# Performance work log

Measured on AMD Instinct MI355X. Metric: run time of the kernel, lower is better.

## Reference

```python
import jax, jax.numpy as jnp
import numpy as np

S, D, H, F = 4096, 2048, 16, 8192
HD = D // H
EPS = 1e-5


def setup_inputs() -> dict:
    key = jax.random.key(0)
    ks = jax.random.split(key, 16)
    sc_d = 1.0 / np.sqrt(D)
    sc_f = 1.0 / np.sqrt(F)
    return {
        "x": jax.random.normal(ks[0], (S, D), dtype=jnp.float32),
        # stacked per-head projections: [H, D, HD]
        "Wq": jax.random.normal(ks[1], (H, D, HD), dtype=jnp.float32) * sc_d,
        "bq": jax.random.normal(ks[2], (H, HD), dtype=jnp.float32) * 0.01,
        "Wk": jax.random.normal(ks[3], (H, D, HD), dtype=jnp.float32) * sc_d,
        "bk": jax.random.normal(ks[4], (H, HD), dtype=jnp.float32) * 0.01,
        "Wv": jax.random.normal(ks[5], (H, D, HD), dtype=jnp.float32) * sc_d,
        "bv": jax.random.normal(ks[6], (H, HD), dtype=jnp.float32) * 0.01,
        "Wp": jax.random.normal(ks[7], (D, D), dtype=jnp.float32) * sc_d,
        "bp": jax.random.normal(ks[8], (D,), dtype=jnp.float32) * 0.01,
        "W1": jax.random.normal(ks[9], (D, F), dtype=jnp.float32) * sc_d,
        "b1": jax.random.normal(ks[10], (F,), dtype=jnp.float32) * 0.01,
        "W2": jax.random.normal(ks[11], (F, D), dtype=jnp.float32) * sc_f,
        "b2": jax.random.normal(ks[12], (D,), dtype=jnp.float32) * 0.01,
        "gamma": jnp.ones((D,), dtype=jnp.float32),
        "beta": jnp.zeros((D,), dtype=jnp.float32),
    }


def _layernorm(x, gamma, beta):
    mu = jnp.mean(x, axis=-1, keepdims=True)
    var = jnp.var(x, axis=-1, keepdims=True)
    return (x - mu) * jax.lax.rsqrt(var + EPS) * gamma + beta


def reference(x, Wq, bq, Wk, bk, Wv, bv, Wp, bp, W1, b1, W2, b2, gamma, beta):
    residual = x
    # batched per-head projections: [H, S, HD]
    q = jnp.einsum('sd,hde->hse', x, Wq) + bq[:, None, :]
    k = jnp.einsum('sd,hde->hse', x, Wk) + bk[:, None, :]
    v = jnp.einsum('sd,hde->hse', x, Wv) + bv[:, None, :]
    scores = jnp.einsum('hse,hte->hst', q, k) / np.sqrt(HD).astype(np.float32)
    attn = jax.nn.softmax(scores, axis=-1)
    heads = jnp.einsum('hst,hte->hse', attn, v)  # [H, S, HD]
    # concat heads along feature dim (head 0 first): [S, H*HD]
    heads = jnp.transpose(heads, (1, 0, 2)).reshape(S, H * HD)
    out = heads @ Wp + bp
    # residual_attn=True, norm_attn=True
    out = out + residual
    out = _layernorm(out, gamma, beta)
    # feedforward (original forward ends here)
    out = jax.nn.relu(out @ W1 + b1) @ W2 + b2
    return out
```

## Files before the change

### kernel.cpp

```cpp
#include <hip/hip_runtime.h>
#include <hip/hip_bf16.h>
#include <cstdint>
#include <cstddef>

#define S 4096
#define D 2048
#define H 16
#define HD 128
#define F 8192

typedef unsigned short ushort_t;
typedef __attribute__((ext_vector_type(8))) short short8;
typedef __attribute__((ext_vector_type(4))) float floatx4;

__device__ __forceinline__ ushort_t f2bf(float f) {
  union { float f; unsigned u; } v; v.f = f;
  unsigned u = v.u;
  return (ushort_t)((u + 0x7fffu + ((u >> 16) & 1u)) >> 16);
}

__device__ __forceinline__ void async16(void* lds, const void* g) {
  __builtin_amdgcn_global_load_lds(
      (const __attribute__((address_space(1))) unsigned int*)g,
      (__attribute__((address_space(3))) unsigned int*)lds, 16, 0, 0);
}

template <int N>
__device__ __forceinline__ void vmcnt_() {
  static_assert(N >= 0 && N <= 4, "vmcnt range");
  if constexpr (N == 0) asm volatile("s_waitcnt vmcnt(0)" ::: "memory");
  else if constexpr (N == 1) asm volatile("s_waitcnt vmcnt(1)" ::: "memory");
  else if constexpr (N == 2) asm volatile("s_waitcnt vmcnt(2)" ::: "memory");
  else if constexpr (N == 3) asm volatile("s_waitcnt vmcnt(3)" ::: "memory");
  else asm volatile("s_waitcnt vmcnt(4)" ::: "memory");
}
__device__ __forceinline__ void bar_() { asm volatile("s_barrier" ::: "memory"); }


__global__ void cast_bf16(const float* __restrict__ src, ushort_t* __restrict__ dst, int n4) {
  int i = blockIdx.x * blockDim.x + threadIdx.x;
  if (i < n4) {
    float4 v = ((const float4*)src)[i];
    ushort4 o;
    o.x = f2bf(v.x); o.y = f2bf(v.y); o.z = f2bf(v.z); o.w = f2bf(v.w);
    ((ushort4*)dst)[i] = o;
  }
}

__global__ void build_bqkv(const float* __restrict__ bq, const float* __restrict__ bk,
                           const float* __restrict__ bv, float* __restrict__ bqkv) {
  int n = blockIdx.x * blockDim.x + threadIdx.x;
  if (n < 3 * D) {
    float v;
    if (n < D) v = bq[n];
    else if (n < 2 * D) v = bk[n - D];
    else v = bv[n - 2 * D];
    bqkv[n] = v;
  }
}

__global__ void transpose_f32_bf16(const float* __restrict__ src, ushort_t* __restrict__ dst,
                                   int ldS, int ldD, long srcBatchStride, long dstBatchRows) {
  __shared__ float t[32][33];
  int b = blockIdx.z;
  src += (size_t)b * srcBatchStride;
  dst += (size_t)b * dstBatchRows * ldD;
  int r0 = blockIdx.x * 32, c0 = blockIdx.y * 32;
  int tx = threadIdx.x, ty = threadIdx.y;
#pragma unroll
  for (int i = 0; i < 4; ++i)
    t[ty + i * 8][tx] = src[(size_t)(r0 + ty + i * 8) * ldS + c0 + tx];
  __syncthreads();
#pragma unroll
  for (int i = 0; i < 4; ++i)
    dst[(size_t)(c0 + ty + i * 8) * ldD + r0 + tx] = f2bf(t[tx][ty + i * 8]);
}

__global__ void transpose_bf16(const ushort_t* __restrict__ src, ushort_t* __restrict__ dst,
                               int ldS, int ldD, int colOff) {
  __shared__ ushort_t t[32][33];
  int r0 = blockIdx.x * 32, c0 = blockIdx.y * 32;
  int tx = threadIdx.x, ty = threadIdx.y;
#pragma unroll
  for (int i = 0; i < 4; ++i)
    t[ty + i * 8][tx] = src[(size_t)(r0 + ty + i * 8) * ldS + colOff + c0 + tx];
  __syncthreads();
#pragma unroll
  for (int i = 0; i < 4; ++i)
    dst[(size_t)(c0 + ty + i * 8) * ldD + r0 + tx] = t[tx][ty + i * 8];
}

template <int MODE, int BM>
__global__ __launch_bounds__(512, 2)
void gemm8p(const ushort_t* __restrict__ A, const ushort_t* __restrict__ Bt,
            const float* __restrict__ bias, const float* __restrict__ resid,
            ushort_t* __restrict__ outb, float* __restrict__ outf,
            int M, int N, int K, int gridN) {
  constexpr int MF = BM / 64;
  constexpr int LA = BM / 128;
  constexpr int AT = BM * 64;
  constexpr int BT = 256 * 64;
  __shared__ __align__(16) ushort_t Abuf[2][AT];
  __shared__ __align__(16) ushort_t Bbuf[2][BT];

  const int tid = threadIdx.x;
  const int l = tid & 63, w = tid >> 6;
  const int c16 = l & 15, g = l >> 4;
  const int wr2 = w >> 2, wc4 = w & 3;

  const int nwg = gridDim.x;
  const int q8 = nwg >> 3, r8 = nwg & 7;
  const int xcd = blockIdx.x & 7, bix = blockIdx.x >> 3;
  const int wgid = (xcd < r8 ? xcd * (q8 + 1) : r8 * (q8 + 1) + (xcd - r8) * q8) + bix;
  const int m0 = (wgid / gridN) * BM;
  const int n0 = (wgid % gridN) * 256;

  const size_t Kb = (size_t)K * 2;

  const char* aSrc[LA]; char* aLds[LA];
#pragma unroll
  for (int i = 0; i < LA; ++i) {
    int ch = i * 512 + tid;
    int row = ch >> 3;
    int slot = ((ch ^ row) & 7) << 4;
    aSrc[i] = (const char*)A + (size_t)(m0 + row) * Kb + slot;
    aLds[i] = (char*)(&Abuf[0][0]) + ch * 16;
  }
  const char* bSrc[2]; char* bLds[2];
#pragma unroll
  for (int i = 0; i < 2; ++i) {
    int ch = i * 512 + tid;
    int row = ch >> 3;
    int slot = ((ch ^ row) & 7) << 4;
    bSrc[i] = (const char*)Bt + (size_t)(n0 + row) * Kb + slot;
    bLds[i] = (char*)(&Bbuf[0][0]) + ch * 16;
  }
  const size_t aHalf = (size_t)(BM / 2) * Kb;
  const size_t bHalf = (size_t)128 * Kb;

  int rdK[2];
  rdK[0] = ((g ^ (c16 & 7)) << 4);
  rdK[1] = (((4 + g) ^ (c16 & 7)) << 4);
  const int aRd = wr2 * (BM / 4) * 128 + c16 * 128;
  const int bRd = wc4 * 32 * 128 + c16 * 128;

  floatx4 acc[2][2][MF][2];
#pragma unroll
  for (int mh = 0; mh < 2; ++mh)
#pragma unroll
    for (int nh = 0; nh < 2; ++nh)
#pragma unroll
      for (int mf = 0; mf < MF; ++mf)
#pragma unroll
        for (int nf = 0; nf < 2; ++nf) acc[mh][nh][mf][nf] = (floatx4){0.f, 0.f, 0.f, 0.f};

  const int NT = K >> 6;

#pragma unroll
  for (int i = 0; i < LA; ++i) async16(aLds[i], aSrc[i]);
#pragma unroll
  for (int i = 0; i < 2; ++i) async16(bLds[i], bSrc[i]);
#pragma unroll
  for (int i = 0; i < 2; ++i) async16(bLds[i] + 128 * 128, bSrc[i] + bHalf);
#pragma unroll
  for (int i = 0; i < LA; ++i) async16(aLds[i] + (BM / 2) * 128, aSrc[i] + aHalf);
  vmcnt_<2 + LA>();
  bar_();

  for (int T = 0; T < NT; ++T) {
    const int kb = T & 1, kn = kb ^ 1;
    const bool last = (T == NT - 1);
    const size_t kOff = (size_t)(T + 1) << 7;
    const char* ab = (const char*)(&Abuf[0][0]) + kb * (AT * 2);
    const char* bb = (const char*)(&Bbuf[0][0]) + kb * (BT * 2);
    const int aOf = kn * (AT * 2), bOf = kn * (BT * 2);
    short8 af[MF][2], bf0[2][2], bf1[2][2];

#pragma unroll
    for (int mf = 0; mf < MF; ++mf)
#pragma unroll
      for (int kk = 0; kk < 2; ++kk)
        af[mf][kk] = *(const short8*)(ab + aRd + mf * 2048 + rdK[kk]);
#pragma unroll
    for (int nf = 0; nf < 2; ++nf)
#pragma unroll
      for (int kk = 0; kk < 2; ++kk)
        bf0[nf][kk] = *(const short8*)(bb + bRd + nf * 2048 + rdK[kk]);
    if (!last) {
#pragma unroll
      for (int i = 0; i < LA; ++i) async16(aLds[i] + aOf, aSrc[i] + kOff);
    }
    bar_();
    __builtin_amdgcn_s_setprio(1);
#pragma unroll
    for (int mf = 0; mf < MF; ++mf)
#pragma unroll
      for (int nf = 0; nf < 2; ++nf)
#pragma unroll
        for (int kk = 0; kk < 2; ++kk)
          acc[0][0][mf][nf] = __builtin_amdgcn_mfma_f32_16x16x32_bf16(
              af[mf][kk], bf0[nf][kk], acc[0][0][mf][nf], 0, 0, 0);
    __builtin_amdgcn_s_setprio(0);
    __builtin_amdgcn_sched_barrier(0);
    if (!last) vmcnt_<2 * LA>(); else vmcnt_<LA>();
    bar_();

#pragma unroll
    for (int nf = 0; nf < 2; ++nf)
#pragma unroll
      for (int kk = 0; kk < 2; ++kk)
        bf1[nf][kk] = *(const short8*)(bb + bRd + 16384 + nf * 2048 + rdK[kk]);
    if (!last) {
#pragma unroll
      for (int i = 0; i < 2; ++i) async16(bLds[i] + bOf, bSrc[i] + kOff);
    }
    bar_();
    __builtin_amdgcn_s_setprio(1);
#pragma unroll
    for (int mf = 0; mf < MF; ++mf)
#pragma unroll
      for (int nf = 0; nf < 2; ++nf)
#pragma unroll
        for (int kk = 0; kk < 2; ++kk)
          acc[0][1][mf][nf] = __builtin_amdgcn_mfma_f32_16x16x32_bf16(
              af[mf][kk], bf1[nf][kk], acc[0][1][mf][nf], 0, 0, 0);
    __builtin_amdgcn_s_setprio(0);
    __builtin_amdgcn_sched_barrier(0);
    if (!last) vmcnt_<LA + 2>(); else vmcnt_<0>();
    bar_();

#pragma unroll
    for (int mf = 0; mf < MF; ++mf)
#pragma unroll
      for (int kk = 0; kk < 2; ++kk)
        af[mf][kk] = *(const short8*)(ab + aRd + (BM / 2) * 128 + mf * 2048 + rdK[kk]);
    if (!last) {
#pragma unroll
      for (int i = 0; i < 2; ++i) async16(bLds[i] + bOf + 16384, bSrc[i] + bHalf + kOff);
    }
    bar_();
    __builtin_amdgcn_s_setprio(1);
#pragma unroll
    for (int mf = 0; mf < MF; ++mf)
#pragma unroll
      for (int nf = 0; nf < 2; ++nf)
#pragma unroll
        for (int kk = 0; kk < 2; ++kk)
          acc[1][1][mf][nf] = __builtin_amdgcn_mfma_f32_16x16x32_bf16(
              af[mf][kk], bf1[nf][kk], acc[1][1][mf][nf], 0, 0, 0);
    __builtin_amdgcn_s_setprio(0);
    __builtin_amdgcn_sched_barrier(0);
    bar_();

    if (!last) {
#pragma unroll
      for (int i = 0; i < LA; ++i) async16(aLds[i] + aOf + (BM / 2) * 128, aSrc[i] + aHalf + kOff);
    }
    bar_();
    __builtin_amdgcn_s_setprio(1);
#pragma unroll
    for (int mf = 0; mf < MF; ++mf)
#pragma unroll
      for (int nf = 0; nf < 2; ++nf)
#pragma unroll
        for (int kk = 0; kk < 2; ++kk)
          acc[1][0][mf][nf] = __builtin_amdgcn_mfma_f32_16x16x32_bf16(
              af[mf][kk], bf0[nf][kk], acc[1][0][mf][nf], 0, 0, 0);
    __builtin_amdgcn_s_setprio(0);
    __builtin_amdgcn_sched_barrier(0);
    if (!last) vmcnt_<2 + LA>();
    bar_();
  }

  const int mBase = m0 + wr2 * (BM / 4) + g * 4;
  const int nBase = n0 + wc4 * 32 + c16;
#pragma unroll
  for (int mh = 0; mh < 2; ++mh)
#pragma unroll
    for (int nh = 0; nh < 2; ++nh)
#pragma unroll
      for (int nf = 0; nf < 2; ++nf) {
        int gcol = nBase + nh * 128 + nf * 16;
        float bj = bias[gcol];
#pragma unroll
        for (int mf = 0; mf < MF; ++mf) {
          int grow = mBase + mh * (BM / 2) + mf * 16;
#pragma unroll
          for (int r = 0; r < 4; ++r) {
            float v = acc[mh][nh][mf][nf][r] + bj;
            size_t o = (size_t)(grow + r) * N + gcol;
            if (MODE == 0) {
              outb[o] = f2bf(v);
            } else if (MODE == 1) {
              outf[o] = v + resid[o];
            } else if (MODE == 2) {
              outb[o] = f2bf(v > 0.f ? v : 0.f);
            } else {
              outf[o] = v;
            }
          }
        }
      }
}

__global__ __launch_bounds__(256, 2)
void attn_kernel(const ushort_t* __restrict__ QKV, const ushort_t* __restrict__ Vt,
                 ushort_t* __restrict__ heads) {
  const int h = blockIdx.y;
  const int tid = threadIdx.x, w = tid >> 6, l = tid & 63;
  const int g = l >> 4, c = l & 15;
  const int q0 = blockIdx.x * 128 + w * 32;
  const float scale = 0.08838834764831845f;

  __shared__ __align__(16) ushort_t Ks[64 * 128];
  __shared__ __align__(16) ushort_t Vs[128 * 64];
  __shared__ __align__(16) ushort_t Ps[4][2][16][72];

  short8 qf[2][4];
#pragma unroll
  for (int u = 0; u < 2; ++u)
#pragma unroll
    for (int k0 = 0; k0 < 4; ++k0)
      qf[u][k0] = *(const short8*)(QKV + (size_t)(q0 + u * 16 + c) * (3 * D) + h * HD + k0 * 32 + g * 8);

  floatx4 o[2][8];
#pragma unroll
  for (int u = 0; u < 2; ++u)
#pragma unroll
    for (int j = 0; j < 8; ++j) o[u][j] = (floatx4){0.f, 0.f, 0.f, 0.f};
  float l_run[2] = {0.f, 0.f};

  for (int t0 = 0; t0 < S; t0 += 64) {
#pragma unroll
    for (int cc = 0; cc < 4; ++cc) {
      int slot = cc * 256 + tid;
      int krow = slot >> 4, kch = slot & 15;
      const char* gk = (const char*)QKV +
          ((size_t)(t0 + krow) * (3 * D) + D + h * HD) * 2 + ((kch ^ (krow & 15)) << 4);
      async16((char*)Ks + (size_t)(cc * 256 + w * 64) * 16, gk);
      int vrow = slot >> 3, vch = slot & 7;
      const char* gv = (const char*)Vt +
          ((size_t)(h * HD + vrow) * S + t0) * 2 + ((vch ^ (vrow & 7)) << 4);
      async16((char*)Vs + (size_t)(cc * 256 + w * 64) * 16, gv);
    }
    __syncthreads();

    floatx4 sc[2][4];
#pragma unroll
    for (int u = 0; u < 2; ++u)
#pragma unroll
      for (int tt = 0; tt < 4; ++tt) sc[u][tt] = (floatx4){0.f, 0.f, 0.f, 0.f};
#pragma unroll
    for (int tt = 0; tt < 4; ++tt) {
      short8 kf[4];
#pragma unroll
      for (int k0 = 0; k0 < 4; ++k0)
        kf[k0] = *(const short8*)(Ks + (tt * 16 + c) * 128 + (((k0 * 4 + g) ^ c) << 3));
#pragma unroll
      for (int u = 0; u < 2; ++u)
#pragma unroll
        for (int k0 = 0; k0 < 4; ++k0)
          sc[u][tt] = __builtin_amdgcn_mfma_f32_16x16x32_bf16(kf[k0], qf[u][k0], sc[u][tt], 0, 0, 0);
    }

#pragma unroll
    for (int u = 0; u < 2; ++u) {
#pragma unroll
      for (int tt = 0; tt < 4; ++tt) {
        float p0 = __expf(sc[u][tt][0] * scale);
        float p1 = __expf(sc[u][tt][1] * scale);
        float p2 = __expf(sc[u][tt][2] * scale);
        float p3 = __expf(sc[u][tt][3] * scale);
        l_run[u] += p0 + p1 + p2 + p3;
        ushort4 pk;
        pk.x = f2bf(p0); pk.y = f2bf(p1); pk.z = f2bf(p2); pk.w = f2bf(p3);
        *reinterpret_cast<ushort4*>(&Ps[w][u][c][tt * 16 + g * 4]) = pk;
      }
    }
    __asm__ volatile("s_waitcnt lgkmcnt(0)" ::: "memory");

    short8 pf[2][2];
#pragma unroll
    for (int u = 0; u < 2; ++u)
#pragma unroll
      for (int tk = 0; tk < 2; ++tk)
        pf[u][tk] = *reinterpret_cast<const short8*>(&Ps[w][u][c][tk * 32 + g * 8]);
#pragma unroll
    for (int j = 0; j < 8; ++j) {
#pragma unroll
      for (int tk = 0; tk < 2; ++tk) {
        short8 vf = *(const short8*)(Vs + (j * 16 + c) * 64 + (((tk * 4 + g) ^ (c & 7)) << 3));
#pragma unroll
        for (int u = 0; u < 2; ++u)
          o[u][j] = __builtin_amdgcn_mfma_f32_16x16x32_bf16(pf[u][tk], vf, o[u][j], 0, 0, 0);
      }
    }
    __syncthreads();
  }

#pragma unroll
  for (int u = 0; u < 2; ++u) {
    float lt = l_run[u];
    lt += __shfl_xor(lt, 16);
    lt += __shfl_xor(lt, 32);
    float linv[4];
#pragma unroll
    for (int r = 0; r < 4; ++r) linv[r] = 1.f / __shfl(lt, g * 4 + r);
    ushort_t* hp = heads + (size_t)(q0 + u * 16 + g * 4) * D + h * HD + c;
#pragma unroll
    for (int j = 0; j < 8; ++j)
#pragma unroll
      for (int r = 0; r < 4; ++r)
        hp[(size_t)r * D + j * 16] = f2bf(o[u][j][r] * linv[r]);
  }
}

__global__ __launch_bounds__(256)
void ln_kernel(const float* __restrict__ preln, const float* __restrict__ gamma,
               const float* __restrict__ beta, ushort_t* __restrict__ y) {
  int row = blockIdx.x, tid = threadIdx.x;
  const float* p = preln + (size_t)row * D;
  float vals[8];
  float sum = 0.f, ss = 0.f;
#pragma unroll
  for (int k = 0; k < 8; ++k) {
    float v = p[tid + k * 256];
    vals[k] = v; sum += v; ss += v * v;
  }
#pragma unroll
  for (int off = 32; off >= 1; off >>= 1) {
    sum += __shfl_xor(sum, off);
    ss += __shfl_xor(ss, off);
  }
  __shared__ float s1[4], s2[4];
  int w = tid >> 6, l = tid & 63;
  if (l == 0) { s1[w] = sum; s2[w] = ss; }
  __syncthreads();
  sum = s1[0] + s1[1] + s1[2] + s1[3];
  ss = s2[0] + s2[1] + s2[2] + s2[3];
  float mu = sum / (float)D;
  float var = ss / (float)D - mu * mu;
  float rs = rsqrtf(var + 1e-5f);
  ushort_t* yr = y + (size_t)row * D;
#pragma unroll
  for (int k = 0; k < 8; ++k) {
    int d = tid + k * 256;
    yr[d] = f2bf((vals[k] - mu) * rs * gamma[d] + beta[d]);
  }
}


extern "C" void kernel_launch(void* const* d_in, const int* in_sizes, int n_in,
                              void* d_out, int out_size, void* d_ws, size_t ws_size,
                              hipStream_t stream) {
  const float* x = (const float*)d_in[0];
  const float* Wq = (const float*)d_in[1];
  const float* bq = (const float*)d_in[2];
  const float* Wk = (const float*)d_in[3];
  const float* bk = (const float*)d_in[4];
  const float* Wv = (const float*)d_in[5];
  const float* bv = (const float*)d_in[6];
  const float* Wp = (const float*)d_in[7];
  const float* bp = (const float*)d_in[8];
  const float* W1 = (const float*)d_in[9];
  const float* b1 = (const float*)d_in[10];
  const float* W2 = (const float*)d_in[11];
  const float* b2 = (const float*)d_in[12];
  const float* gamma = (const float*)d_in[13];
  const float* beta = (const float*)d_in[14];

  char* ws = (char*)d_ws;
  ushort_t* WQKVT = (ushort_t*)(ws + 0);
  ushort_t* XB    = (ushort_t*)(ws + 25165824);
  float*    BQKV  = (float*)(ws + 41943040);
  ushort_t* WPT   = (ushort_t*)(ws + 41975808);
  ushort_t* W1T   = (ushort_t*)(ws + 50364416);
  ushort_t* W2T   = (ushort_t*)(ws + 83918848);
  ushort_t* QKV   = (ushort_t*)(ws + 117473280);
  ushort_t* HEADS = (ushort_t*)(ws + 167804928);
  ushort_t* VT    = (ushort_t*)(ws + 184582144);
  float*    PRELN = (float*)(ws + 0);
  ushort_t* AB    = (ushort_t*)(ws + 117473280);
  ushort_t* Y     = (ushort_t*)(ws + 184582144);
  float* OUT = (float*)d_out;

  dim3 tb(32, 8);
  cast_bf16<<<(S * D / 4 + 255) / 256, 256, 0, stream>>>(x, XB, S * D / 4);
  build_bqkv<<<(3 * D + 255) / 256, 256, 0, stream>>>(bq, bk, bv, BQKV);
  transpose_f32_bf16<<<dim3(D / 32, HD / 32, H), tb, 0, stream>>>(Wq, WQKVT, HD, D, (long)D * HD, HD);
  transpose_f32_bf16<<<dim3(D / 32, HD / 32, H), tb, 0, stream>>>(Wk, WQKVT + (size_t)D * D, HD, D, (long)D * HD, HD);
  transpose_f32_bf16<<<dim3(D / 32, HD / 32, H), tb, 0, stream>>>(Wv, WQKVT + (size_t)2 * D * D, HD, D, (long)D * HD, HD);
  transpose_f32_bf16<<<dim3(D / 32, D / 32, 1), tb, 0, stream>>>(Wp, WPT, D, D, 0, 0);
  transpose_f32_bf16<<<dim3(D / 32, F / 32, 1), tb, 0, stream>>>(W1, W1T, F, D, 0, 0);
  transpose_f32_bf16<<<dim3(F / 32, D / 32, 1), tb, 0, stream>>>(W2, W2T, D, F, 0, 0);
  gemm8p<0, 256><<<dim3((S / 256) * (3 * D / 256)), 512, 0, stream>>>(
      XB, WQKVT, BQKV, nullptr, QKV, nullptr, S, 3 * D, D, 3 * D / 256);
  transpose_bf16<<<dim3(S / 32, D / 32), tb, 0, stream>>>(QKV, VT, 3 * D, S, 2 * D);
  attn_kernel<<<dim3(S / 128, H), 256, 0, stream>>>(QKV, VT, HEADS);
  gemm8p<1, 128><<<dim3((S / 128) * (D / 256)), 512, 0, stream>>>(
      HEADS, WPT, bp, x, nullptr, PRELN, S, D, D, D / 256);
  ln_kernel<<<S, 256, 0, stream>>>(PRELN, gamma, beta, Y);
  gemm8p<2, 256><<<dim3((S / 256) * (F / 256)), 512, 0, stream>>>(
      Y, W1T, b1, nullptr, AB, nullptr, S, F, D, F / 256);
  gemm8p<3, 128><<<dim3((S / 128) * (D / 256)), 512, 0, stream>>>(
      AB, W2T, b2, nullptr, nullptr, OUT, S, D, F, D / 256);
}
```

Baseline: 959.0 us.

## Restructure bf16 GEMM main loop into two-tile unrolled deeper prefetch pipeline

Rewrites the gemm8p main loop to process two K-tiles per iteration with both LDS buffers preloaded up front. Each quarter-tile region is refilled from global memory for tile k+2 as soon as its fragments are read into registers, which lengthens the prefetch distance and is meant to hide global load latency. Explicit lgkmcnt(0) waits with scheduling barriers are added before each MFMA block. The extra waits and barriers could cost some issue overlap, and the loop now assumes K is a multiple of 128.

```diff
diff --git a/kernel.cpp b/kernel.cpp
--- a/kernel.cpp
+++ b/kernel.cpp
@@ -27,14 +27,22 @@
 
 template <int N>
 __device__ __forceinline__ void vmcnt_() {
-  static_assert(N >= 0 && N <= 4, "vmcnt range");
+  static_assert(N >= 0 && N <= 8, "vmcnt range");
   if constexpr (N == 0) asm volatile("s_waitcnt vmcnt(0)" ::: "memory");
   else if constexpr (N == 1) asm volatile("s_waitcnt vmcnt(1)" ::: "memory");
   else if constexpr (N == 2) asm volatile("s_waitcnt vmcnt(2)" ::: "memory");
   else if constexpr (N == 3) asm volatile("s_waitcnt vmcnt(3)" ::: "memory");
-  else asm volatile("s_waitcnt vmcnt(4)" ::: "memory");
+  else if constexpr (N == 4) asm volatile("s_waitcnt vmcnt(4)" ::: "memory");
+  else if constexpr (N == 5) asm volatile("s_waitcnt vmcnt(5)" ::: "memory");
+  else if constexpr (N == 6) asm volatile("s_waitcnt vmcnt(6)" ::: "memory");
+  else if constexpr (N == 7) asm volatile("s_waitcnt vmcnt(7)" ::: "memory");
+  else asm volatile("s_waitcnt vmcnt(8)" ::: "memory");
 }
 __device__ __forceinline__ void bar_() { asm volatile("s_barrier" ::: "memory"); }
+__device__ __forceinline__ void lgkm0_() {
+  asm volatile("s_waitcnt lgkmcnt(0)" ::: "memory");
+  __builtin_amdgcn_sched_barrier(0);
+}
 
 
 __global__ void cast_bf16(const float* __restrict__ src, ushort_t* __restrict__ dst, int n4) {
@@ -96,17 +104,15 @@
             const float* __restrict__ bias, const float* __restrict__ resid,
             ushort_t* __restrict__ outb, float* __restrict__ outf,
             int M, int N, int K, int gridN) {
-  constexpr int MF = BM / 64;
+  constexpr int MQ = BM / 64;
   constexpr int LA = BM / 128;
-  constexpr int AT = BM * 64;
-  constexpr int BT = 256 * 64;
-  __shared__ __align__(16) ushort_t Abuf[2][AT];
-  __shared__ __align__(16) ushort_t Bbuf[2][BT];
+  __shared__ __align__(16) ushort_t Abuf[2][BM * 64];
+  __shared__ __align__(16) ushort_t Bbuf[2][256 * 64];
 
   const int tid = threadIdx.x;
   const int l = tid & 63, w = tid >> 6;
   const int c16 = l & 15, g = l >> 4;
-  const int wr2 = w >> 2, wc4 = w & 3;
+  const int wm = w >> 2, wn = w & 3;
 
   const int nwg = gridDim.x;
   const int q8 = nwg >> 3, r8 = nwg & 7;
@@ -116,14 +122,15 @@
   const int n0 = (wgid % gridN) * 256;
 
   const size_t Kb = (size_t)K * 2;
+  const size_t aHalfB = (size_t)(BM / 2) * Kb;
+  const size_t bHalfB = (size_t)128 * Kb;
 
   const char* aSrc[LA]; char* aLds[LA];
 #pragma unroll
   for (int i = 0; i < LA; ++i) {
     int ch = i * 512 + tid;
     int row = ch >> 3;
-    int slot = ((ch ^ row) & 7) << 4;
-    aSrc[i] = (const char*)A + (size_t)(m0 + row) * Kb + slot;
+    aSrc[i] = (const char*)A + (size_t)(m0 + row) * Kb + (((ch ^ row) & 7) << 4);
     aLds[i] = (char*)(&Abuf[0][0]) + ch * 16;
   }
   const char* bSrc[2]; char* bLds[2];
@@ -131,163 +138,149 @@
   for (int i = 0; i < 2; ++i) {
     int ch = i * 512 + tid;
     int row = ch >> 3;
-    int slot = ((ch ^ row) & 7) << 4;
-    bSrc[i] = (const char*)Bt + (size_t)(n0 + row) * Kb + slot;
+    bSrc[i] = (const char*)Bt + (size_t)(n0 + row) * Kb + (((ch ^ row) & 7) << 4);
     bLds[i] = (char*)(&Bbuf[0][0]) + ch * 16;
   }
-  const size_t aHalf = (size_t)(BM / 2) * Kb;
-  const size_t bHalf = (size_t)128 * Kb;
+
+  auto stA = [&](int p, int h, int kByte) {
+#pragma unroll
+    for (int i = 0; i < LA; ++i)
+      async16(aLds[i] + p * (BM * 128) + h * (BM * 64), aSrc[i] + (size_t)h * aHalfB + kByte);
+  };
+  auto stB = [&](int p, int h, int kByte) {
+#pragma unroll
+    for (int i = 0; i < 2; ++i)
+      async16(bLds[i] + p * 32768 + h * 16384, bSrc[i] + (size_t)h * bHalfB + kByte);
+  };
 
   int rdK[2];
   rdK[0] = ((g ^ (c16 & 7)) << 4);
   rdK[1] = (((4 + g) ^ (c16 & 7)) << 4);
-  const int aRd = wr2 * (BM / 4) * 128 + c16 * 128;
-  const int bRd = wc4 * 32 * 128 + c16 * 128;
-
-  floatx4 acc[2][2][MF][2];
-#pragma unroll
-  for (int mh = 0; mh < 2; ++mh)
-#pragma unroll
-    for (int nh = 0; nh < 2; ++nh)
-#pragma unroll
-      for (int mf = 0; mf < MF; ++mf)
-#pragma unroll
-        for (int nf = 0; nf < 2; ++nf) acc[mh][nh][mf][nf] = (floatx4){0.f, 0.f, 0.f, 0.f};
-
-  const int NT = K >> 6;
-
-#pragma unroll
-  for (int i = 0; i < LA; ++i) async16(aLds[i], aSrc[i]);
-#pragma unroll
-  for (int i = 0; i < 2; ++i) async16(bLds[i], bSrc[i]);
-#pragma unroll
-  for (int i = 0; i < 2; ++i) async16(bLds[i] + 128 * 128, bSrc[i] + bHalf);
-#pragma unroll
-  for (int i = 0; i < LA; ++i) async16(aLds[i] + (BM / 2) * 128, aSrc[i] + aHalf);
-  vmcnt_<2 + LA>();
+  const char* Ab0 = (const char*)(&Abuf[0][0]);
+  const char* Ab1 = Ab0 + BM * 128;
+  const char* Bb0 = (const char*)(&Bbuf[0][0]);
+  const char* Bb1 = Bb0 + 32768;
+
+  floatx4 acc[2][2][MQ][2];
+#pragma unroll
+  for (int ah = 0; ah < 2; ++ah)
+#pragma unroll
+    for (int bh = 0; bh < 2; ++bh)
+#pragma unroll
+      for (int mf = 0; mf < MQ; ++mf)
+#pragma unroll
+        for (int nf = 0; nf < 2; ++nf) acc[ah][bh][mf][nf] = (floatx4){0.f, 0.f, 0.f, 0.f};
+
+  short8 af[MQ][2], bf0[2][2], bf1[2][2];
+  auto ldA = [&](const char* base, int h) {
+#pragma unroll
+    for (int mf = 0; mf < MQ; ++mf)
+#pragma unroll
+      for (int kk = 0; kk < 2; ++kk)
+        af[mf][kk] = *(const short8*)(base + h * (BM * 64) +
+            (wm * (BM / 4) + mf * 16 + c16) * 128 + rdK[kk]);
+  };
+  auto ldB = [&](const char* base, int h, short8 (&bf)[2][2]) {
+#pragma unroll
+    for (int nf = 0; nf < 2; ++nf)
+#pragma unroll
+      for (int kk = 0; kk < 2; ++kk)
+        bf[nf][kk] = *(const short8*)(base + h * 16384 +
+            (wn * 32 + nf * 16 + c16) * 128 + rdK[kk]);
+  };
+  auto mmaQ = [&](int ah, int bh, short8 (&bf)[2][2]) {
+    __builtin_amdgcn_s_setprio(1);
+#pragma unroll
+    for (int mf = 0; mf < MQ; ++mf)
+#pragma unroll
+      for (int nf = 0; nf < 2; ++nf)
+#pragma unroll
+        for (int kk = 0; kk < 2; ++kk)
+          acc[ah][bh][mf][nf] = __builtin_amdgcn_mfma_f32_16x16x32_bf16(
+              af[mf][kk], bf[nf][kk], acc[ah][bh][mf][nf], 0, 0, 0);
+    __builtin_amdgcn_s_setprio(0);
+  };
+
+  stA(0, 0, 0); stB(0, 0, 0); stB(0, 1, 0); stA(0, 1, 0);
+  stA(1, 0, 128); stB(1, 0, 128); stB(1, 1, 128);
+  vmcnt_<LA + 4>();
   bar_();
 
-  for (int T = 0; T < NT; ++T) {
-    const int kb = T & 1, kn = kb ^ 1;
-    const bool last = (T == NT - 1);
-    const size_t kOff = (size_t)(T + 1) << 7;
-    const char* ab = (const char*)(&Abuf[0][0]) + kb * (AT * 2);
-    const char* bb = (const char*)(&Bbuf[0][0]) + kb * (BT * 2);
-    const int aOf = kn * (AT * 2), bOf = kn * (BT * 2);
-    short8 af[MF][2], bf0[2][2], bf1[2][2];
-
-#pragma unroll
-    for (int mf = 0; mf < MF; ++mf)
-#pragma unroll
-      for (int kk = 0; kk < 2; ++kk)
-        af[mf][kk] = *(const short8*)(ab + aRd + mf * 2048 + rdK[kk]);
-#pragma unroll
-    for (int nf = 0; nf < 2; ++nf)
-#pragma unroll
-      for (int kk = 0; kk < 2; ++kk)
-        bf0[nf][kk] = *(const short8*)(bb + bRd + nf * 2048 + rdK[kk]);
-    if (!last) {
-#pragma unroll
-      for (int i = 0; i < LA; ++i) async16(aLds[i] + aOf, aSrc[i] + kOff);
-    }
-    bar_();
-    __builtin_amdgcn_s_setprio(1);
-#pragma unroll
-    for (int mf = 0; mf < MF; ++mf)
-#pragma unroll
-      for (int nf = 0; nf < 2; ++nf)
-#pragma unroll
-        for (int kk = 0; kk < 2; ++kk)
-          acc[0][0][mf][nf] = __builtin_amdgcn_mfma_f32_16x16x32_bf16(
-              af[mf][kk], bf0[nf][kk], acc[0][0][mf][nf], 0, 0, 0);
-    __builtin_amdgcn_s_setprio(0);
-    __builtin_amdgcn_sched_barrier(0);
-    if (!last) vmcnt_<2 * LA>(); else vmcnt_<LA>();
-    bar_();
-
-#pragma unroll
-    for (int nf = 0; nf < 2; ++nf)
-#pragma unroll
-      for (int kk = 0; kk < 2; ++kk)
-        bf1[nf][kk] = *(const short8*)(bb + bRd + 16384 + nf * 2048 + rdK[kk]);
-    if (!last) {
-#pragma unroll
-      for (int i = 0; i < 2; ++i) async16(bLds[i] + bOf, bSrc[i] + kOff);
-    }
-    bar_();
-    __builtin_amdgcn_s_setprio(1);
-#pragma unroll
-    for (int mf = 0; mf < MF; ++mf)
-#pragma unroll
-      for (int nf = 0; nf < 2; ++nf)
-#pragma unroll
-        for (int kk = 0; kk < 2; ++kk)
-          acc[0][1][mf][nf] = __builtin_amdgcn_mfma_f32_16x16x32_bf16(
-              af[mf][kk], bf1[nf][kk], acc[0][1][mf][nf], 0, 0, 0);
-    __builtin_amdgcn_s_setprio(0);
-    __builtin_amdgcn_sched_barrier(0);
-    if (!last) vmcnt_<LA + 2>(); else vmcnt_<0>();
-    bar_();
-
-#pragma unroll
-    for (int mf = 0; mf < MF; ++mf)
-#pragma unroll
-      for (int kk = 0; kk < 2; ++kk)
-        af[mf][kk] = *(const short8*)(ab + aRd + (BM / 2) * 128 + mf * 2048 + rdK[kk]);
-    if (!last) {
-#pragma unroll
-      for (int i = 0; i < 2; ++i) async16(bLds[i] + bOf + 16384, bSrc[i] + bHalf + kOff);
-    }
-    bar_();
-    __builtin_amdgcn_s_setprio(1);
-#pragma unroll
-    for (int mf = 0; mf < MF; ++mf)
-#pragma unroll
-      for (int nf = 0; nf < 2; ++nf)
-#pragma unroll
-        for (int kk = 0; kk < 2; ++kk)
-          acc[1][1][mf][nf] = __builtin_amdgcn_mfma_f32_16x16x32_bf16(
-              af[mf][kk], bf1[nf][kk], acc[1][1][mf][nf], 0, 0, 0);
-    __builtin_amdgcn_s_setprio(0);
-    __builtin_amdgcn_sched_barrier(0);
-    bar_();
-
-    if (!last) {
-#pragma unroll
-      for (int i = 0; i < LA; ++i) async16(aLds[i] + aOf + (BM / 2) * 128, aSrc[i] + aHalf + kOff);
-    }
-    bar_();
-    __builtin_amdgcn_s_setprio(1);
-#pragma unroll
-    for (int mf = 0; mf < MF; ++mf)
-#pragma unroll
-      for (int nf = 0; nf < 2; ++nf)
-#pragma unroll
-        for (int kk = 0; kk < 2; ++kk)
-          acc[1][0][mf][nf] = __builtin_amdgcn_mfma_f32_16x16x32_bf16(
-              af[mf][kk], bf0[nf][kk], acc[1][0][mf][nf], 0, 0, 0);
-    __builtin_amdgcn_s_setprio(0);
-    __builtin_amdgcn_sched_barrier(0);
-    if (!last) vmcnt_<2 + LA>();
-    bar_();
-  }
-
-  const int mBase = m0 + wr2 * (BM / 4) + g * 4;
-  const int nBase = n0 + wc4 * 32 + c16;
-#pragma unroll
-  for (int mh = 0; mh < 2; ++mh)
-#pragma unroll
-    for (int nh = 0; nh < 2; ++nh)
+  const int NI = K >> 7;
+  for (int i = 0; i < NI; ++i) {
+    const bool lastI = (i == NI - 1);
+    const int kE = i << 8;
+
+    ldA(Ab0, 0); ldB(Bb0, 0, bf0);
+    stA(1, 1, kE + 128);
+    bar_(); lgkm0_();
+    mmaQ(0, 0, bf0);
+    __builtin_amdgcn_sched_barrier(0);
+    bar_();
+
+    ldB(Bb0, 1, bf1);
+    if (!lastI) stA(0, 0, kE + 256);
+    bar_(); lgkm0_();
+    mmaQ(0, 1, bf1);
+    __builtin_amdgcn_sched_barrier(0);
+    bar_();
+
+    ldA(Ab0, 1);
+    if (!lastI) stB(0, 0, kE + 256);
+    bar_(); lgkm0_();
+    mmaQ(1, 1, bf1);
+    __builtin_amdgcn_sched_barrier(0);
+    bar_();
+
+    if (!lastI) stB(0, 1, kE + 256);
+    bar_(); lgkm0_();
+    mmaQ(1, 0, bf0);
+    __builtin_amdgcn_sched_barrier(0);
+    if (lastI) vmcnt_<0>(); else vmcnt_<LA + 4>();
+    bar_();
+
+    ldA(Ab1, 0); ldB(Bb1, 0, bf0);
+    if (!lastI) stA(0, 1, kE + 256);
+    bar_(); lgkm0_();
+    mmaQ(0, 0, bf0);
+    __builtin_amdgcn_sched_barrier(0);
+    bar_();
+
+    ldB(Bb1, 1, bf1);
+    if (!lastI) stA(1, 0, kE + 384);
+    bar_(); lgkm0_();
+    mmaQ(0, 1, bf1);
+    __builtin_amdgcn_sched_barrier(0);
+    bar_();
+
+    ldA(Ab1, 1);
+    if (!lastI) stB(1, 0, kE + 384);
+    bar_(); lgkm0_();
+    mmaQ(1, 1, bf1);
+    __builtin_amdgcn_sched_barrier(0);
+    bar_();
+
+    if (!lastI) stB(1, 1, kE + 384);
+    bar_(); lgkm0_();
+    mmaQ(1, 0, bf0);
+    __builtin_amdgcn_sched_barrier(0);
+    if (!lastI) { vmcnt_<LA + 4>(); bar_(); }
+  }
+
+#pragma unroll
+  for (int ah = 0; ah < 2; ++ah)
+#pragma unroll
+    for (int bh = 0; bh < 2; ++bh)
 #pragma unroll
       for (int nf = 0; nf < 2; ++nf) {
-        int gcol = nBase + nh * 128 + nf * 16;
+        int gcol = n0 + bh * 128 + wn * 32 + nf * 16 + c16;
         float bj = bias[gcol];
 #pragma unroll
-        for (int mf = 0; mf < MF; ++mf) {
-          int grow = mBase + mh * (BM / 2) + mf * 16;
+        for (int mf = 0; mf < MQ; ++mf) {
+          int grow = m0 + ah * (BM / 2) + wm * (BM / 4) + mf * 16 + g * 4;
 #pragma unroll
           for (int r = 0; r < 4; ++r) {
-            float v = acc[mh][nh][mf][nf][r] + bj;
+            float v = acc[ah][bh][mf][nf][r] + bj;
             size_t o = (size_t)(grow + r) * N + gcol;
             if (MODE == 0) {
               outb[o] = f2bf(v);
```

Result: no change. 956.2 us (-0.3%).
